# Kernel optimization log

Hardware: AMD Instinct MI355X
Metric: run time of the kernel (lower is better)

The kernel has to match this reference:

```python
import jax, jax.numpy as jnp
import numpy as np
from jax import lax

N = 10000
T_CTX = 24
HORIZON = 40
T = T_CTX + HORIZON  # 64
N_ENV = 17
COORD = 2
N_IN = N_ENV + COORD + 2  # 21
H = 128


def _lstm_cell(inp, h, c, Wih, Whh, bih, bhh):
    # torch.nn.LSTMCell gate order: input, forget, cell, output
    g = inp @ Wih.T + bih + h @ Whh.T + bhh  # [N, 4H]
    i, f, gg, o = jnp.split(g, 4, axis=1)
    c2 = jax.nn.sigmoid(f) * c + jax.nn.sigmoid(i) * jnp.tanh(gg)
    h2 = jax.nn.sigmoid(o) * jnp.tanh(c2)
    return h2, c2


def setup_inputs() -> dict:
    key = jax.random.key(0)
    ks = jax.random.split(key, 30)
    kaiming = lambda k, shp: jax.random.normal(k, shp, jnp.float32) * np.sqrt(2.0 / shp[-1]).astype(np.float32)
    u = 1.0 / np.sqrt(H).astype(np.float32)
    uni = lambda k, shp: jax.random.uniform(k, shp, jnp.float32, -u, u)
    inp = {
        'x': jax.random.uniform(ks[0], (N, T), jnp.float32),
        'coords': jax.random.normal(ks[1], (N, COORD), jnp.float32),
        'env': jax.random.normal(ks[2], (N, N_ENV, T), jnp.float32),
        'areas': jax.random.uniform(ks[3], (N,), jnp.float32),
        # encoder params (2 stacked H->H LSTM layers)
        'W_enc_in': kaiming(ks[4], (H, N_IN)),
        'enc_Wih': uni(ks[5], (2, 4 * H, H)),
        'enc_Whh': uni(ks[6], (2, 4 * H, H)),
        'enc_bih': uni(ks[7], (2, 4 * H)),
        'enc_bhh': uni(ks[8], (2, 4 * H)),
        # decoder NodeLSTM params
        'W_dec_in': kaiming(ks[9], (H, N_IN)),
        'in_Wih': uni(ks[10], (4 * H, 2 * H)),  # lstm_in takes [proj, enc_state]
        'in_Whh': uni(ks[11], (4 * H, H)),
        'in_bih': uni(ks[12], (4 * H,)),
        'in_bhh': uni(ks[13], (4 * H,)),
        'd_Wih': uni(ks[14], (4 * H, H)),
        'd_Whh': uni(ks[15], (4 * H, H)),
        'd_bih': uni(ks[16], (4 * H,)),
        'd_bhh': uni(ks[17], (4 * H,)),
        # SourceSinkMLP params
        'mlp_W1': kaiming(ks[18], (H, H + N_IN)),
        'mlp_b1': jnp.zeros((H,), jnp.float32),
        'mlp_W2': kaiming(ks[19], (2, H)),
        'mlp_b2': jnp.zeros((2,), jnp.float32),
    }
    return inp


def reference(x, coords, env, areas, W_enc_in, enc_Wih, enc_Whh, enc_bih, enc_bhh,
              W_dec_in, in_Wih, in_Whh, in_bih, in_bhh, d_Wih, d_Whh, d_bih, d_bhh,
              mlp_W1, mlp_b1, mlp_W2, mlp_b2):
    n = x.shape[0]
    areas_c = areas[:, None]
    x_seq = x.T                              # [T, N]
    env_seq = jnp.transpose(env, (2, 0, 1))  # [T, N, N_ENV]
    z = jnp.zeros((n, H), x.dtype)

    # ---- RecurrentEncoder over context steps ----
    def enc_step(carry, xs):
        h0, c0, h1, c1 = carry
        xt, et = xs
        inp = jnp.concatenate([xt[:, None], coords, et, areas_c], axis=1)  # [N, N_IN]
        proj = inp @ W_enc_in.T
        h0, c0 = _lstm_cell(proj, h0, c0, enc_Wih[0], enc_Whh[0], enc_bih[0], enc_bhh[0])
        h1, c1 = _lstm_cell(h0, h1, c1, enc_Wih[1], enc_Whh[1], enc_bih[1], enc_bhh[1])
        return (h0, c0, h1, c1), None

    (h0, c0, h1, c1), _ = lax.scan(enc_step, (z, z, z, z), (x_seq[:T_CTX], env_seq[:T_CTX]))
    enc_state = h1  # captured once in setup_states, constant over the forecast

    # ---- NodeLSTM + SourceSinkMLP rollout over the horizon ----
    def dec_step(carry, et):
        xc, h0, c0, h1, c1 = carry  # xc: [N, 1]
        inp = jnp.concatenate([xc, coords, et, areas_c], axis=1)  # [N, N_IN]
        proj = jnp.concatenate([inp @ W_dec_in.T, enc_state], axis=1)  # [N, 2H]
        h0, c0 = _lstm_cell(proj, h0, c0, in_Wih, in_Whh, in_bih, in_bhh)
        h1, c1 = _lstm_cell(h0, h1, c1, d_Wih, d_Whh, d_bih, d_bhh)
        # SourceSinkMLP
        zmid = jax.nn.leaky_relu(jnp.concatenate([h1, inp], axis=1) @ mlp_W1.T + mlp_b1)
        ss = zmid @ mlp_W2.T + mlp_b2  # [N, 2]
        source = jax.nn.sigmoid(ss[:, :1])
        sink = jax.nn.sigmoid(ss[:, 1:2]) * xc
        xn = xc + source - sink
        return (xn, h0, c0, h1, c1), xn[:, 0]

    x0 = x[:, T_CTX - 1][:, None]
    _, ys = lax.scan(dec_step, (x0, h0, c0, h1, c1), env_seq[T_CTX:T_CTX + HORIZON])
    return ys.T  # [N, HORIZON]
```

## Files before the change

### kernel.cpp

```cpp
#include <hip/hip_runtime.h>

#define NTOT  10000
#define TALL  64
#define TCTX  24
#define HOR   40
#define HH    128
#define G4    512
#define NENV  17
#define SAMP  16

typedef __attribute__((ext_vector_type(8))) short  bf16x8;
typedef __attribute__((ext_vector_type(4))) float  f32x4;
typedef unsigned short u16;

#define SEG_W0E   0
#define SEG_W0D   8192
#define SEG_WIH1  16384
#define SEG_WHH1  24576
#define SEG_DWIH  32768
#define SEG_DWHH  40960
#define SEG_M0E   49152
#define SEG_MDE   51200
#define SEG_WIHH  53248
#define SEG_W1H   61440
#define SEG_W1I   63488
#define NFRAGS    64000

#define L_WLDS  0
#define L_H0    131072
#define L_H1    135424
#define L_ZMS   139776
#define L_INPS  144128
#define L_XBLK  145408
#define L_W2L   146944
#define L_XCS   147968
#define SMEM_TOTAL 148032

__device__ __forceinline__ float sigf(float v)   { return 1.0f/(1.0f + __expf(-v)); }
__device__ __forceinline__ float tanhf_(float v) { return 1.0f - 2.0f/(__expf(2.0f*v) + 1.0f); }
__device__ __forceinline__ u16 f2bf(float f){
    unsigned int u = __float_as_uint(f);
    u += 0x7fffu + ((u >> 16) & 1u);
    return (u16)(u >> 16);
}
__device__ __forceinline__ float bf2f(u16 h){ return __uint_as_float(((unsigned int)h) << 16); }

__global__ void fold_kernel(const float* __restrict__ enc_Wih, const float* __restrict__ enc_Whh,
                            const float* __restrict__ W_enc_in,
                            const float* __restrict__ in_Wih,  const float* __restrict__ in_Whh,
                            const float* __restrict__ W_dec_in,
                            const float* __restrict__ dWih,    const float* __restrict__ dWhh,
                            const float* __restrict__ mlp_W1,  const float* __restrict__ mlp_b1,
                            const float* __restrict__ enc_bih, const float* __restrict__ enc_bhh,
                            const float* __restrict__ in_bih,  const float* __restrict__ in_bhh,
                            void* __restrict__ ws)
{
    int fid = blockIdx.x*256 + threadIdx.x;
    if (fid >= NFRAGS) return;
    const int lane = fid & 63;
    const int cc = lane & 15;
    const int kg = lane >> 4;
    float vals[8];

    if (fid < 49152) {
        int segi = fid >> 13;
        int loc  = fid & 8191;
        int gt   = loc >> 8;
        int kb   = (loc >> 6) & 3;
        int r    = gt*16 + cc;
        int k0   = kb*32 + kg*8;
        const float* src;
        switch (segi) {
            case 0: src = enc_Whh;          break;
            case 1: src = in_Whh;           break;
            case 2: src = enc_Wih + 65536;  break;
            case 3: src = enc_Whh + 65536;  break;
            case 4: src = dWih;             break;
            default: src = dWhh;            break;
        }
        #pragma unroll
        for (int j = 0; j < 8; ++j) vals[j] = src[(size_t)r*128 + k0 + j];
    } else if (fid < 53248) {
        int loc = fid - 49152;
        int which = loc >> 11; loc &= 2047;
        int gt = loc >> 6;
        int r  = gt*16 + cc;
        int k0 = kg*8;
        const float* A = which ? (in_Wih + (size_t)r*256) : (enc_Wih + (size_t)r*128);
        const float* B = which ? W_dec_in : W_enc_in;
        float bias = which ? (in_bih[r] + in_bhh[r]) : (enc_bih[r] + enc_bhh[r]);
        #pragma unroll
        for (int j = 0; j < 8; ++j) {
            int k = k0 + j;
            float v = 0.f;
            int c = (k <= 16) ? (3 + k) : (k == 17 ? 0 : (k == 18 ? 1 : (k == 19 ? 2 : (k == 20 ? 20 : -1))));
            if (k == 21) v = bias;
            else if (c >= 0) {
                float a = 0.f;
                for (int h = 0; h < HH; ++h) a = fmaf(A[h], B[h*21 + c], a);
                v = a;
            }
            vals[j] = v;
        }
    } else if (fid < 61440) {
        int loc = fid - 53248;
        int gt = loc >> 8; int kb = (loc >> 6) & 3;
        int r = gt*16 + cc; int k0 = kb*32 + kg*8;
        #pragma unroll
        for (int j = 0; j < 8; ++j) vals[j] = in_Wih[(size_t)r*256 + 128 + k0 + j];
    } else if (fid < 63488) {
        int loc = fid - 61440;
        int gt = loc >> 8; int kb = (loc >> 6) & 3;
        int r = gt*16 + cc; int k0 = kb*32 + kg*8;
        #pragma unroll
        for (int j = 0; j < 8; ++j) vals[j] = mlp_W1[(size_t)r*149 + k0 + j];
    } else {
        int loc = fid - 63488;
        int gt = loc >> 6;
        int r = gt*16 + cc; int k0 = kg*8;
        #pragma unroll
        for (int j = 0; j < 8; ++j) {
            int k = k0 + j; float v = 0.f;
            if (k <= 16)      v = mlp_W1[(size_t)r*149 + 131 + k];
            else if (k == 17) v = mlp_W1[(size_t)r*149 + 128];
            else if (k == 18) v = mlp_W1[(size_t)r*149 + 129];
            else if (k == 19) v = mlp_W1[(size_t)r*149 + 130];
            else if (k == 20) v = mlp_W1[(size_t)r*149 + 148];
            else if (k == 21) v = mlp_b1[r];
            vals[j] = v;
        }
    }
    union { uint4 u4; u16 us[8]; } pk;
    #pragma unroll
    for (int j = 0; j < 8; ++j) pk.us[j] = f2bf(vals[j]);
    *(uint4*)((char*)ws + (size_t)fid*16) = pk.u4;
}

__global__ __launch_bounds__(256, 1)
void lstm_main(const float* __restrict__ x, const float* __restrict__ coords,
               const float* __restrict__ env, const float* __restrict__ areas,
               const float* __restrict__ enc_bih, const float* __restrict__ enc_bhh,
               const float* __restrict__ dbih,   const float* __restrict__ dbhh,
               const float* __restrict__ mlp_W2, const float* __restrict__ mlp_b2,
               const void* __restrict__ ws, float* __restrict__ out)
{
    extern __shared__ char smem[];
    u16*   WLDS = (u16*)(smem + L_WLDS);
    u16*   h0s  = (u16*)(smem + L_H0);
    u16*   h1s  = (u16*)(smem + L_H1);
    u16*   zms  = (u16*)(smem + L_ZMS);
    u16*   inps = (u16*)(smem + L_INPS);
    float* xblk = (float*)(smem + L_XBLK);
    float* w2l  = (float*)(smem + L_W2L);
    float* xcs  = (float*)(smem + L_XCS);

    const int tid  = threadIdx.x;
    const int lane = tid & 63;
    const int wid  = tid >> 6;
    const int cc   = lane & 15;
    const int kg   = lane >> 4;
    const int s0   = blockIdx.x * SAMP;
    const char* wsb = (const char*)ws;

    int gmap[8];
    #pragma unroll
    for (int m = 0; m < 8; ++m) gmap[m] = ((m >> 1) << 3) + (wid << 1) + (m & 1);

    #pragma unroll 4
    for (int it = 0; it < 32; ++it) {
        int idx = it*256 + tid;
        ((uint4*)WLDS)[idx] = ((const uint4*)wsb)[idx];
    }
    for (int it = 0; it < 9; ++it) {
        int idx = it*256 + tid;
        if (idx < 2176) { h0s[idx] = 0; h1s[idx] = 0; }
    }
    #pragma unroll
    for (int rep = 0; rep < 2; ++rep) {
        int idx = rep*256 + tid;
        if (idx < 384) xblk[idx] = x[(size_t)(s0 + idx/24)*TALL + (idx % 24)];
    }
    w2l[tid] = mlp_W2[tid];

    const int sA = tid / NENV, eA = tid - sA*NENV;
    const int iB = tid + 256;
    const int sB = iB / NENV, eB = iB - sB*NENV;
    const float* envpA = env + ((size_t)(s0 + sA)*NENV + eA)*TALL;
    const float* envpB = env + ((size_t)(s0 + ((tid < 16) ? sB : 0))*NENV + ((tid < 16) ? eB : 0))*TALL;

    if (tid < SAMP) {
        inps[tid*40 + 18] = f2bf(coords[(size_t)(s0+tid)*2 + 0]);
        inps[tid*40 + 19] = f2bf(coords[(size_t)(s0+tid)*2 + 1]);
        inps[tid*40 + 20] = f2bf(areas[s0+tid]);
        inps[tid*40 + 21] = 0x3F80;
        #pragma unroll
        for (int c = 22; c < 32; ++c) inps[tid*40 + c] = 0;
    }

    bf16x8 WrA[32], WrB[32], MdB[8], W1HB[8], W1IB[2];
    float  lb1[8];
    #pragma unroll
    for (int m = 0; m < 8; ++m) {
        int gt = gmap[m];
        #pragma unroll
        for (int kb = 0; kb < 4; ++kb) {
            WrA[m*4+kb] = *(const bf16x8*)(wsb + ((size_t)(SEG_WIH1 + (gt*4+kb)*64 + lane))*16);
            WrB[m*4+kb] = *(const bf16x8*)(wsb + ((size_t)(SEG_WHH1 + (gt*4+kb)*64 + lane))*16);
        }
        MdB[m] = *(const bf16x8*)(wsb + ((size_t)(SEG_M0E + gt*64 + lane))*16);
        int grow = gt*16 + cc;
        lb1[m] = enc_bih[512 + grow] + enc_bhh[512 + grow];
    }

    float c0r[8], c1r[8];
    #pragma unroll
    for (int i = 0; i < 8; ++i) { c0r[i] = 0.f; c1r[i] = 0.f; }

    float evA = envpA[0];
    float evB = (tid < 16) ? envpB[0] : 0.f;
    __syncthreads();

    const f32x4 zero4 = {0.f, 0.f, 0.f, 0.f};

    #pragma unroll 1
    for (int t = 0; t < TCTX; ++t) {
        inps[sA*40 + eA] = f2bf(evA);
        if (tid < 16) { inps[sB*40 + eB] = f2bf(evB); inps[tid*40 + 17] = f2bf(xblk[tid*24 + t]); }
        __syncthreads();
        if (t + 1 < TALL) { evA = envpA[t+1]; if (tid < 16) evB = envpB[t+1]; }

        bf16x8 ia = *(const bf16x8*)(inps + cc*40 + kg*8);
        f32x4 acc[8];
        #pragma unroll
        for (int m = 0; m < 8; ++m)
            acc[m] = __builtin_amdgcn_mfma_f32_16x16x32_bf16(ia, MdB[m], zero4, 0, 0, 0);
        #pragma unroll
        for (int kb = 0; kb < 4; ++kb) {
            bf16x8 ha = *(const bf16x8*)(h0s + cc*136 + kb*32 + kg*8);
            #pragma unroll
            for (int m = 0; m < 8; ++m) {
                bf16x8 wb = *(const bf16x8*)((char*)WLDS + ((size_t)((gmap[m]*4+kb)*64 + lane))*16);
                acc[m] = __builtin_amdgcn_mfma_f32_16x16x32_bf16(ha, wb, acc[m], 0, 0, 0);
            }
        }
        float h2[8];
        #pragma unroll
        for (int ut = 0; ut < 2; ++ut)
        #pragma unroll
        for (int r = 0; r < 4; ++r) {
            float gi = acc[0+ut][r], gf = acc[2+ut][r], gg = acc[4+ut][r], go = acc[6+ut][r];
            float c2 = fmaf(sigf(gf), c0r[ut*4+r], sigf(gi)*tanhf_(gg));
            c0r[ut*4+r] = c2;
            h2[ut*4+r] = sigf(go)*tanhf_(c2);
        }
        __syncthreads();
        #pragma unroll
        for (int ut = 0; ut < 2; ++ut)
        #pragma unroll
        for (int r = 0; r < 4; ++r)
            h0s[(kg*4+r)*136 + wid*32 + ut*16 + cc] = f2bf(h2[ut*4+r]);
        __syncthreads();

        #pragma unroll
        for (int m = 0; m < 8; ++m) { f32x4 v = {lb1[m], lb1[m], lb1[m], lb1[m]}; acc[m] = v; }
        #pragma unroll
        for (int kb = 0; kb < 4; ++kb) {
            bf16x8 ha = *(const bf16x8*)(h0s + cc*136 + kb*32 + kg*8);
            #pragma unroll
            for (int m = 0; m < 8; ++m)
                acc[m] = __builtin_amdgcn_mfma_f32_16x16x32_bf16(ha, WrA[m*4+kb], acc[m], 0, 0, 0);
        }
        #pragma unroll
        for (int kb = 0; kb < 4; ++kb) {
            bf16x8 ha = *(const bf16x8*)(h1s + cc*136 + kb*32 + kg*8);
            #pragma unroll
            for (int m = 0; m < 8; ++m)
                acc[m] = __builtin_amdgcn_mfma_f32_16x16x32_bf16(ha, WrB[m*4+kb], acc[m], 0, 0, 0);
        }
        #pragma unroll
        for (int ut = 0; ut < 2; ++ut)
        #pragma unroll
        for (int r = 0; r < 4; ++r) {
            float gi = acc[0+ut][r], gf = acc[2+ut][r], gg = acc[4+ut][r], go = acc[6+ut][r];
            float c2 = fmaf(sigf(gf), c1r[ut*4+r], sigf(gi)*tanhf_(gg));
            c1r[ut*4+r] = c2;
            h2[ut*4+r] = sigf(go)*tanhf_(c2);
        }
        __syncthreads();
        #pragma unroll
        for (int ut = 0; ut < 2; ++ut)
        #pragma unroll
        for (int r = 0; r < 4; ++r)
            h1s[(kg*4+r)*136 + wid*32 + ut*16 + cc] = f2bf(h2[ut*4+r]);
    }

    __syncthreads();

    f32x4 baseD[8];
    #pragma unroll
    for (int m = 0; m < 8; ++m) baseD[m] = zero4;
    #pragma unroll
    for (int kb = 0; kb < 4; ++kb) {
        bf16x8 ha = *(const bf16x8*)(h1s + cc*136 + kb*32 + kg*8);
        #pragma unroll
        for (int m = 0; m < 8; ++m) {
            bf16x8 wb = *(const bf16x8*)(wsb + ((size_t)(SEG_WIHH + (gmap[m]*4+kb)*64 + lane))*16);
            baseD[m] = __builtin_amdgcn_mfma_f32_16x16x32_bf16(ha, wb, baseD[m], 0, 0, 0);
        }
    }
    #pragma unroll
    for (int m = 0; m < 8; ++m) {
        int gt = gmap[m];
        #pragma unroll
        for (int kb = 0; kb < 4; ++kb) {
            WrA[m*4+kb] = *(const bf16x8*)(wsb + ((size_t)(SEG_DWIH + (gt*4+kb)*64 + lane))*16);
            WrB[m*4+kb] = *(const bf16x8*)(wsb + ((size_t)(SEG_DWHH + (gt*4+kb)*64 + lane))*16);
        }
        MdB[m] = *(const bf16x8*)(wsb + ((size_t)(SEG_MDE + gt*64 + lane))*16);
        int grow = gt*16 + cc;
        lb1[m] = dbih[grow] + dbhh[grow];
    }
    #pragma unroll
    for (int uu = 0; uu < 2; ++uu) {
        int mt = (wid << 1) + uu;
        #pragma unroll
        for (int kb = 0; kb < 4; ++kb)
            W1HB[uu*4+kb] = *(const bf16x8*)(wsb + ((size_t)(SEG_W1H + (mt*4+kb)*64 + lane))*16);
        W1IB[uu] = *(const bf16x8*)(wsb + ((size_t)(SEG_W1I + mt*64 + lane))*16);
    }
    #pragma unroll 4
    for (int it = 0; it < 32; ++it) {
        int idx = it*256 + tid;
        ((uint4*)WLDS)[idx] = ((const uint4*)(wsb + (size_t)SEG_W0D*16))[idx];
    }
    if (tid < SAMP) {
        float xv = xblk[tid*24 + 23];
        xcs[tid] = xv;
        inps[tid*40 + 17] = f2bf(xv);
    }
    const float b20 = mlp_b2[0], b21 = mlp_b2[1];
    const int hs = lane >> 2, hq = lane & 3;
    __syncthreads();

    #pragma unroll 1
    for (int td = 0; td < HOR; ++td) {
        const int t = TCTX + td;
        inps[sA*40 + eA] = f2bf(evA);
        if (tid < 16) inps[sB*40 + eB] = f2bf(evB);
        __syncthreads();
        float xch = xcs[hs];
        if (t + 1 < TALL) { evA = envpA[t+1]; if (tid < 16) evB = envpB[t+1]; }

        bf16x8 ia = *(const bf16x8*)(inps + cc*40 + kg*8);
        f32x4 acc[8];
        #pragma unroll
        for (int m = 0; m < 8; ++m)
            acc[m] = __builtin_amdgcn_mfma_f32_16x16x32_bf16(ia, MdB[m], baseD[m], 0, 0, 0);
        #pragma unroll
        for (int kb = 0; kb < 4; ++kb) {
            bf16x8 ha = *(const bf16x8*)(h0s + cc*136 + kb*32 + kg*8);
            #pragma unroll
            for (int m = 0; m < 8; ++m) {
                bf16x8 wb = *(const bf16x8*)((char*)WLDS + ((size_t)((gmap[m]*4+kb)*64 + lane))*16);
                acc[m] = __builtin_amdgcn_mfma_f32_16x16x32_bf16(ha, wb, acc[m], 0, 0, 0);
            }
        }
        float h2[8];
        #pragma unroll
        for (int ut = 0; ut < 2; ++ut)
        #pragma unroll
        for (int r = 0; r < 4; ++r) {
            float gi = acc[0+ut][r], gf = acc[2+ut][r], gg = acc[4+ut][r], go = acc[6+ut][r];
            float c2 = fmaf(sigf(gf), c0r[ut*4+r], sigf(gi)*tanhf_(gg));
            c0r[ut*4+r] = c2;
            h2[ut*4+r] = sigf(go)*tanhf_(c2);
        }
        __syncthreads();
        #pragma unroll
        for (int ut = 0; ut < 2; ++ut)
        #pragma unroll
        for (int r = 0; r < 4; ++r)
            h0s[(kg*4+r)*136 + wid*32 + ut*16 + cc] = f2bf(h2[ut*4+r]);
        __syncthreads();

        #pragma unroll
        for (int m = 0; m < 8; ++m) { f32x4 v = {lb1[m], lb1[m], lb1[m], lb1[m]}; acc[m] = v; }
        #pragma unroll
        for (int kb = 0; kb < 4; ++kb) {
            bf16x8 ha = *(const bf16x8*)(h0s + cc*136 + kb*32 + kg*8);
            #pragma unroll
            for (int m = 0; m < 8; ++m)
                acc[m] = __builtin_amdgcn_mfma_f32_16x16x32_bf16(ha, WrA[m*4+kb], acc[m], 0, 0, 0);
        }
        #pragma unroll
        for (int kb = 0; kb < 4; ++kb) {
            bf16x8 ha = *(const bf16x8*)(h1s + cc*136 + kb*32 + kg*8);
            #pragma unroll
            for (int m = 0; m < 8; ++m)
                acc[m] = __builtin_amdgcn_mfma_f32_16x16x32_bf16(ha, WrB[m*4+kb], acc[m], 0, 0, 0);
        }
        #pragma unroll
        for (int ut = 0; ut < 2; ++ut)
        #pragma unroll
        for (int r = 0; r < 4; ++r) {
            float gi = acc[0+ut][r], gf = acc[2+ut][r], gg = acc[4+ut][r], go = acc[6+ut][r];
            float c2 = fmaf(sigf(gf), c1r[ut*4+r], sigf(gi)*tanhf_(gg));
            c1r[ut*4+r] = c2;
            h2[ut*4+r] = sigf(go)*tanhf_(c2);
        }
        __syncthreads();
        #pragma unroll
        for (int ut = 0; ut < 2; ++ut)
        #pragma unroll
        for (int r = 0; r < 4; ++r)
            h1s[(kg*4+r)*136 + wid*32 + ut*16 + cc] = f2bf(h2[ut*4+r]);
        __syncthreads();

        f32x4 macc[2];
        #pragma unroll
        for (int uu = 0; uu < 2; ++uu)
            macc[uu] = __builtin_amdgcn_mfma_f32_16x16x32_bf16(ia, W1IB[uu], zero4, 0, 0, 0);
        #pragma unroll
        for (int kb = 0; kb < 4; ++kb) {
            bf16x8 ha = *(const bf16x8*)(h1s + cc*136 + kb*32 + kg*8);
            #pragma unroll
            for (int uu = 0; uu < 2; ++uu)
                macc[uu] = __builtin_amdgcn_mfma_f32_16x16x32_bf16(ha, W1HB[uu*4+kb], macc[uu], 0, 0, 0);
        }
        #pragma unroll
        for (int uu = 0; uu < 2; ++uu)
        #pragma unroll
        for (int r = 0; r < 4; ++r) {
            float z = macc[uu][r];
            z = (z > 0.f) ? z : 0.01f*z;
            zms[(kg*4+r)*136 + wid*32 + uu*16 + cc] = f2bf(z);
        }
        __syncthreads();

        float a0 = 0.f, a1 = 0.f;
        #pragma unroll
        for (int c8 = 0; c8 < 4; ++c8) {
            bf16x8 z8 = *(const bf16x8*)(zms + hs*136 + hq*32 + c8*8);
            #pragma unroll
            for (int j = 0; j < 8; ++j) {
                float zf = bf2f((u16)z8[j]);
                int u = hq*32 + c8*8 + j;
                a0 = fmaf(zf, w2l[u], a0);
                a1 = fmaf(zf, w2l[128 + u], a1);
            }
        }
        a0 += __shfl_xor(a0, 1); a0 += __shfl_xor(a0, 2);
        a1 += __shfl_xor(a1, 1); a1 += __shfl_xor(a1, 2);
        float xn = xch + sigf(a0 + b20) - sigf(a1 + b21)*xch;
        if (wid == 0 && hq == 0) {
            xcs[hs] = xn;
            inps[hs*40 + 17] = f2bf(xn);
            out[(size_t)(s0 + hs)*HOR + td] = xn;
        }
    }
}

extern "C" void kernel_launch(void* const* d_in, const int* in_sizes, int n_in,
                              void* d_out, int out_size, void* d_ws, size_t ws_size,
                              hipStream_t stream)
{
    const float* x        = (const float*)d_in[0];
    const float* coords   = (const float*)d_in[1];
    const float* env      = (const float*)d_in[2];
    const float* areas    = (const float*)d_in[3];
    const float* W_enc_in = (const float*)d_in[4];
    const float* enc_Wih  = (const float*)d_in[5];
    const float* enc_Whh  = (const float*)d_in[6];
    const float* enc_bih  = (const float*)d_in[7];
    const float* enc_bhh  = (const float*)d_in[8];
    const float* W_dec_in = (const float*)d_in[9];
    const float* in_Wih   = (const float*)d_in[10];
    const float* in_Whh   = (const float*)d_in[11];
    const float* in_bih   = (const float*)d_in[12];
    const float* in_bhh   = (const float*)d_in[13];
    const float* dWih     = (const float*)d_in[14];
    const float* dWhh     = (const float*)d_in[15];
    const float* dbih     = (const float*)d_in[16];
    const float* dbhh     = (const float*)d_in[17];
    const float* mlp_W1   = (const float*)d_in[18];
    const float* mlp_b1   = (const float*)d_in[19];
    const float* mlp_W2   = (const float*)d_in[20];
    const float* mlp_b2   = (const float*)d_in[21];
    float* out = (float*)d_out;

    fold_kernel<<<dim3(250), dim3(256), 0, stream>>>(
        enc_Wih, enc_Whh, W_enc_in, in_Wih, in_Whh, W_dec_in,
        dWih, dWhh, mlp_W1, mlp_b1, enc_bih, enc_bhh, in_bih, in_bhh, d_ws);

    hipFuncSetAttribute((const void*)lstm_main,
                        hipFuncAttributeMaxDynamicSharedMemorySize, SMEM_TOTAL);
    lstm_main<<<dim3(NTOT/SAMP), dim3(256), SMEM_TOTAL, stream>>>(
        x, coords, env, areas, enc_bih, enc_bhh, dbih, dbhh, mlp_W2, mlp_b2, d_ws, out);
    (void)in_sizes; (void)n_in; (void)out_size; (void)ws_size;
}
```

Before: 1.200 ms.

## Split LSTM gate tiles across eight waves and double-buffer hidden states

```diff
diff --git a/kernel.cpp b/kernel.cpp
--- a/kernel.cpp
+++ b/kernel.cpp
@@ -26,15 +26,18 @@
 #define SEG_W1I   63488
 #define NFRAGS    64000
 
-#define L_WLDS  0
-#define L_H0    131072
-#define L_H1    135424
-#define L_ZMS   139776
-#define L_INPS  144128
-#define L_XBLK  145408
-#define L_W2L   146944
-#define L_XCS   147968
-#define SMEM_TOTAL 148032
+#define L_MDL   0
+#define L_W1H   32768
+#define L_W1I   65536
+#define L_BASE  73728
+#define L_H0    106496
+#define L_H1    115200
+#define L_ZMS   123904
+#define L_INPS  128256
+#define L_XBLK  129536
+#define L_W2L   131072
+#define L_XCS   132096
+#define SMEM_TOTAL 132160
 
 __device__ __forceinline__ float sigf(float v)   { return 1.0f/(1.0f + __expf(-v)); }
 __device__ __forceinline__ float tanhf_(float v) { return 1.0f - 2.0f/(__expf(2.0f*v) + 1.0f); }
@@ -136,7 +139,7 @@
     *(uint4*)((char*)ws + (size_t)fid*16) = pk.u4;
 }
 
-__global__ __launch_bounds__(256, 1)
+__global__ __launch_bounds__(512, 2)
 void lstm_main(const float* __restrict__ x, const float* __restrict__ coords,
                const float* __restrict__ env, const float* __restrict__ areas,
                const float* __restrict__ enc_bih, const float* __restrict__ enc_bhh,
@@ -145,9 +148,10 @@
                const void* __restrict__ ws, float* __restrict__ out)
 {
     extern __shared__ char smem[];
-    u16*   WLDS = (u16*)(smem + L_WLDS);
-    u16*   h0s  = (u16*)(smem + L_H0);
-    u16*   h1s  = (u16*)(smem + L_H1);
+    u16*   MdL  = (u16*)(smem + L_MDL);
+    u16*   W1Hl = (u16*)(smem + L_W1H);
+    u16*   W1Il = (u16*)(smem + L_W1I);
+    float* baseL= (float*)(smem + L_BASE);
     u16*   zms  = (u16*)(smem + L_ZMS);
     u16*   inps = (u16*)(smem + L_INPS);
     float* xblk = (float*)(smem + L_XBLK);
@@ -161,33 +165,20 @@
     const int kg   = lane >> 4;
     const int s0   = blockIdx.x * SAMP;
     const char* wsb = (const char*)ws;
-
-    int gmap[8];
+    const f32x4 zero4 = {0.f, 0.f, 0.f, 0.f};
+
     #pragma unroll
-    for (int m = 0; m < 8; ++m) gmap[m] = ((m >> 1) << 3) + (wid << 1) + (m & 1);
-
-    #pragma unroll 4
-    for (int it = 0; it < 32; ++it) {
-        int idx = it*256 + tid;
-        ((uint4*)WLDS)[idx] = ((const uint4*)wsb)[idx];
-    }
-    for (int it = 0; it < 9; ++it) {
-        int idx = it*256 + tid;
-        if (idx < 2176) { h0s[idx] = 0; h1s[idx] = 0; }
-    }
-    #pragma unroll
-    for (int rep = 0; rep < 2; ++rep) {
-        int idx = rep*256 + tid;
-        if (idx < 384) xblk[idx] = x[(size_t)(s0 + idx/24)*TALL + (idx % 24)];
-    }
-    w2l[tid] = mlp_W2[tid];
-
-    const int sA = tid / NENV, eA = tid - sA*NENV;
-    const int iB = tid + 256;
-    const int sB = iB / NENV, eB = iB - sB*NENV;
-    const float* envpA = env + ((size_t)(s0 + sA)*NENV + eA)*TALL;
-    const float* envpB = env + ((size_t)(s0 + ((tid < 16) ? sB : 0))*NENV + ((tid < 16) ? eB : 0))*TALL;
-
+    for (int i = 0; i < 4; ++i) {
+        ((uint4*)(smem + L_MDL))[i*512 + tid] = ((const uint4*)wsb)[SEG_M0E + i*512 + tid];
+        ((uint4*)(smem + L_W1H))[i*512 + tid] = ((const uint4*)wsb)[SEG_W1H + i*512 + tid];
+    }
+    ((uint4*)(smem + L_W1I))[tid] = ((const uint4*)wsb)[SEG_W1I + tid];
+    for (int i = tid; i < 2176; i += 512) {
+        ((u16*)(smem + L_H0 + 4352))[i] = 0;
+        ((u16*)(smem + L_H1 + 4352))[i] = 0;
+    }
+    if (tid < 384) xblk[tid] = x[(size_t)(s0 + tid/24)*TALL + (tid % 24)];
+    if (tid < 256) w2l[tid] = mlp_W2[tid];
     if (tid < SAMP) {
         inps[tid*40 + 18] = f2bf(coords[(size_t)(s0+tid)*2 + 0]);
         inps[tid*40 + 19] = f2bf(coords[(size_t)(s0+tid)*2 + 1]);
@@ -197,142 +188,130 @@
         for (int c = 22; c < 32; ++c) inps[tid*40 + c] = 0;
     }
 
-    bf16x8 WrA[32], WrB[32], MdB[8], W1HB[8], W1IB[2];
-    float  lb1[8];
+    const int sA = tid / NENV, eA = tid - sA*NENV;
+    const bool envth = (tid < 272);
+    const float* envp = env + ((size_t)(s0 + (envth ? sA : 0))*NENV + (envth ? eA : 0))*TALL;
+    float evA = envth ? envp[0] : 0.f;
+
+    bf16x8 W0r[16], WrA[16], WrB[16];
+    float  lb1[4];
     #pragma unroll
-    for (int m = 0; m < 8; ++m) {
-        int gt = gmap[m];
-        #pragma unroll
-        for (int kb = 0; kb < 4; ++kb) {
-            WrA[m*4+kb] = *(const bf16x8*)(wsb + ((size_t)(SEG_WIH1 + (gt*4+kb)*64 + lane))*16);
-            WrB[m*4+kb] = *(const bf16x8*)(wsb + ((size_t)(SEG_WHH1 + (gt*4+kb)*64 + lane))*16);
-        }
-        MdB[m] = *(const bf16x8*)(wsb + ((size_t)(SEG_M0E + gt*64 + lane))*16);
+    for (int g = 0; g < 4; ++g) {
+        int gt = g*8 + wid;
+        #pragma unroll
+        for (int kb = 0; kb < 4; ++kb) {
+            W0r[g*4+kb] = *(const bf16x8*)(wsb + ((size_t)(SEG_W0E  + (gt*4+kb)*64 + lane))*16);
+            WrA[g*4+kb] = *(const bf16x8*)(wsb + ((size_t)(SEG_WIH1 + (gt*4+kb)*64 + lane))*16);
+            WrB[g*4+kb] = *(const bf16x8*)(wsb + ((size_t)(SEG_WHH1 + (gt*4+kb)*64 + lane))*16);
+        }
         int grow = gt*16 + cc;
-        lb1[m] = enc_bih[512 + grow] + enc_bhh[512 + grow];
-    }
-
-    float c0r[8], c1r[8];
-    #pragma unroll
-    for (int i = 0; i < 8; ++i) { c0r[i] = 0.f; c1r[i] = 0.f; }
-
-    float evA = envpA[0];
-    float evB = (tid < 16) ? envpB[0] : 0.f;
+        lb1[g] = enc_bih[512 + grow] + enc_bhh[512 + grow];
+    }
+
+    float c0r[4] = {0.f,0.f,0.f,0.f};
+    float c1r[4] = {0.f,0.f,0.f,0.f};
     __syncthreads();
-
-    const f32x4 zero4 = {0.f, 0.f, 0.f, 0.f};
 
     #pragma unroll 1
     for (int t = 0; t < TCTX; ++t) {
-        inps[sA*40 + eA] = f2bf(evA);
-        if (tid < 16) { inps[sB*40 + eB] = f2bf(evB); inps[tid*40 + 17] = f2bf(xblk[tid*24 + t]); }
-        __syncthreads();
-        if (t + 1 < TALL) { evA = envpA[t+1]; if (tid < 16) evB = envpB[t+1]; }
+        u16* h0w = (u16*)(smem + L_H0 + (t&1)*4352);
+        u16* h0r = (u16*)(smem + L_H0 + ((t&1)^1)*4352);
+        u16* h1w = (u16*)(smem + L_H1 + (t&1)*4352);
+        u16* h1r = (u16*)(smem + L_H1 + ((t&1)^1)*4352);
+
+        if (envth)    inps[sA*40 + eA]  = f2bf(evA);
+        if (tid < 16) inps[tid*40 + 17] = f2bf(xblk[tid*24 + t]);
+        __syncthreads();
+        if (envth && t+1 < TALL) evA = envp[t+1];
 
         bf16x8 ia = *(const bf16x8*)(inps + cc*40 + kg*8);
-        f32x4 acc[8];
-        #pragma unroll
-        for (int m = 0; m < 8; ++m)
-            acc[m] = __builtin_amdgcn_mfma_f32_16x16x32_bf16(ia, MdB[m], zero4, 0, 0, 0);
-        #pragma unroll
-        for (int kb = 0; kb < 4; ++kb) {
-            bf16x8 ha = *(const bf16x8*)(h0s + cc*136 + kb*32 + kg*8);
-            #pragma unroll
-            for (int m = 0; m < 8; ++m) {
-                bf16x8 wb = *(const bf16x8*)((char*)WLDS + ((size_t)((gmap[m]*4+kb)*64 + lane))*16);
-                acc[m] = __builtin_amdgcn_mfma_f32_16x16x32_bf16(ha, wb, acc[m], 0, 0, 0);
+        f32x4 acc[4];
+        #pragma unroll
+        for (int g = 0; g < 4; ++g) {
+            bf16x8 md = *(const bf16x8*)(MdL + ((size_t)((g*8+wid)*64 + lane))*8);
+            acc[g] = __builtin_amdgcn_mfma_f32_16x16x32_bf16(ia, md, zero4, 0, 0, 0);
+        }
+        #pragma unroll
+        for (int kb = 0; kb < 4; ++kb) {
+            bf16x8 ha = *(const bf16x8*)(h0r + cc*136 + kb*32 + kg*8);
+            #pragma unroll
+            for (int g = 0; g < 4; ++g)
+                acc[g] = __builtin_amdgcn_mfma_f32_16x16x32_bf16(ha, W0r[g*4+kb], acc[g], 0, 0, 0);
+        }
+        float h2[4];
+        #pragma unroll
+        for (int r = 0; r < 4; ++r) {
+            float c2 = fmaf(sigf(acc[1][r]), c0r[r], sigf(acc[0][r])*tanhf_(acc[2][r]));
+            c0r[r] = c2;
+            h2[r] = sigf(acc[3][r])*tanhf_(c2);
+        }
+        #pragma unroll
+        for (int r = 0; r < 4; ++r)
+            h0w[(kg*4+r)*136 + wid*16 + cc] = f2bf(h2[r]);
+        __syncthreads();
+
+        #pragma unroll
+        for (int g = 0; g < 4; ++g) { f32x4 v = {lb1[g],lb1[g],lb1[g],lb1[g]}; acc[g] = v; }
+        #pragma unroll
+        for (int kb = 0; kb < 4; ++kb) {
+            bf16x8 ha = *(const bf16x8*)(h0w + cc*136 + kb*32 + kg*8);
+            #pragma unroll
+            for (int g = 0; g < 4; ++g)
+                acc[g] = __builtin_amdgcn_mfma_f32_16x16x32_bf16(ha, WrA[g*4+kb], acc[g], 0, 0, 0);
+        }
+        #pragma unroll
+        for (int kb = 0; kb < 4; ++kb) {
+            bf16x8 ha = *(const bf16x8*)(h1r + cc*136 + kb*32 + kg*8);
+            #pragma unroll
+            for (int g = 0; g < 4; ++g)
+                acc[g] = __builtin_amdgcn_mfma_f32_16x16x32_bf16(ha, WrB[g*4+kb], acc[g], 0, 0, 0);
+        }
+        #pragma unroll
+        for (int r = 0; r < 4; ++r) {
+            float c2 = fmaf(sigf(acc[1][r]), c1r[r], sigf(acc[0][r])*tanhf_(acc[2][r]));
+            c1r[r] = c2;
+            h2[r] = sigf(acc[3][r])*tanhf_(c2);
+        }
+        #pragma unroll
+        for (int r = 0; r < 4; ++r)
+            h1w[(kg*4+r)*136 + wid*16 + cc] = f2bf(h2[r]);
+    }
+
+    __syncthreads();
+
+    {
+        u16* hEnc = (u16*)(smem + L_H1 + 4352);
+        f32x4 bD[4];
+        #pragma unroll
+        for (int g = 0; g < 4; ++g) bD[g] = zero4;
+        #pragma unroll
+        for (int kb = 0; kb < 4; ++kb) {
+            bf16x8 ha = *(const bf16x8*)(hEnc + cc*136 + kb*32 + kg*8);
+            #pragma unroll
+            for (int g = 0; g < 4; ++g) {
+                bf16x8 wb = *(const bf16x8*)(wsb + ((size_t)(SEG_WIHH + ((g*8+wid)*4+kb)*64 + lane))*16);
+                bD[g] = __builtin_amdgcn_mfma_f32_16x16x32_bf16(ha, wb, bD[g], 0, 0, 0);
             }
         }
-        float h2[8];
-        #pragma unroll
-        for (int ut = 0; ut < 2; ++ut)
-        #pragma unroll
-        for (int r = 0; r < 4; ++r) {
-            float gi = acc[0+ut][r], gf = acc[2+ut][r], gg = acc[4+ut][r], go = acc[6+ut][r];
-            float c2 = fmaf(sigf(gf), c0r[ut*4+r], sigf(gi)*tanhf_(gg));
-            c0r[ut*4+r] = c2;
-            h2[ut*4+r] = sigf(go)*tanhf_(c2);
-        }
-        __syncthreads();
-        #pragma unroll
-        for (int ut = 0; ut < 2; ++ut)
-        #pragma unroll
-        for (int r = 0; r < 4; ++r)
-            h0s[(kg*4+r)*136 + wid*32 + ut*16 + cc] = f2bf(h2[ut*4+r]);
-        __syncthreads();
-
-        #pragma unroll
-        for (int m = 0; m < 8; ++m) { f32x4 v = {lb1[m], lb1[m], lb1[m], lb1[m]}; acc[m] = v; }
-        #pragma unroll
-        for (int kb = 0; kb < 4; ++kb) {
-            bf16x8 ha = *(const bf16x8*)(h0s + cc*136 + kb*32 + kg*8);
-            #pragma unroll
-            for (int m = 0; m < 8; ++m)
-                acc[m] = __builtin_amdgcn_mfma_f32_16x16x32_bf16(ha, WrA[m*4+kb], acc[m], 0, 0, 0);
-        }
-        #pragma unroll
-        for (int kb = 0; kb < 4; ++kb) {
-            bf16x8 ha = *(const bf16x8*)(h1s + cc*136 + kb*32 + kg*8);
-            #pragma unroll
-            for (int m = 0; m < 8; ++m)
-                acc[m] = __builtin_amdgcn_mfma_f32_16x16x32_bf16(ha, WrB[m*4+kb], acc[m], 0, 0, 0);
-        }
-        #pragma unroll
-        for (int ut = 0; ut < 2; ++ut)
-        #pragma unroll
-        for (int r = 0; r < 4; ++r) {
-            float gi = acc[0+ut][r], gf = acc[2+ut][r], gg = acc[4+ut][r], go = acc[6+ut][r];
-            float c2 = fmaf(sigf(gf), c1r[ut*4+r], sigf(gi)*tanhf_(gg));
-            c1r[ut*4+r] = c2;
-            h2[ut*4+r] = sigf(go)*tanhf_(c2);
-        }
-        __syncthreads();
-        #pragma unroll
-        for (int ut = 0; ut < 2; ++ut)
-        #pragma unroll
-        for (int r = 0; r < 4; ++r)
-            h1s[(kg*4+r)*136 + wid*32 + ut*16 + cc] = f2bf(h2[ut*4+r]);
-    }
-
-    __syncthreads();
-
-    f32x4 baseD[8];
+        #pragma unroll
+        for (int g = 0; g < 4; ++g)
+            *(f32x4*)(baseL + ((size_t)((wid*4+g)*64 + lane))*4) = bD[g];
+    }
     #pragma unroll
-    for (int m = 0; m < 8; ++m) baseD[m] = zero4;
+    for (int g = 0; g < 4; ++g) {
+        int gt = g*8 + wid;
+        #pragma unroll
+        for (int kb = 0; kb < 4; ++kb) {
+            W0r[g*4+kb] = *(const bf16x8*)(wsb + ((size_t)(SEG_W0D  + (gt*4+kb)*64 + lane))*16);
+            WrA[g*4+kb] = *(const bf16x8*)(wsb + ((size_t)(SEG_DWIH + (gt*4+kb)*64 + lane))*16);
+            WrB[g*4+kb] = *(const bf16x8*)(wsb + ((size_t)(SEG_DWHH + (gt*4+kb)*64 + lane))*16);
+        }
+        int grow = gt*16 + cc;
+        lb1[g] = dbih[grow] + dbhh[grow];
+    }
     #pragma unroll
-    for (int kb = 0; kb < 4; ++kb) {
-        bf16x8 ha = *(const bf16x8*)(h1s + cc*136 + kb*32 + kg*8);
-        #pragma unroll
-        for (int m = 0; m < 8; ++m) {
-            bf16x8 wb = *(const bf16x8*)(wsb + ((size_t)(SEG_WIHH + (gmap[m]*4+kb)*64 + lane))*16);
-            baseD[m] = __builtin_amdgcn_mfma_f32_16x16x32_bf16(ha, wb, baseD[m], 0, 0, 0);
-        }
-    }
-    #pragma unroll
-    for (int m = 0; m < 8; ++m) {
-        int gt = gmap[m];
-        #pragma unroll
-        for (int kb = 0; kb < 4; ++kb) {
-            WrA[m*4+kb] = *(const bf16x8*)(wsb + ((size_t)(SEG_DWIH + (gt*4+kb)*64 + lane))*16);
-            WrB[m*4+kb] = *(const bf16x8*)(wsb + ((size_t)(SEG_DWHH + (gt*4+kb)*64 + lane))*16);
-        }
-        MdB[m] = *(const bf16x8*)(wsb + ((size_t)(SEG_MDE + gt*64 + lane))*16);
-        int grow = gt*16 + cc;
-        lb1[m] = dbih[grow] + dbhh[grow];
-    }
-    #pragma unroll
-    for (int uu = 0; uu < 2; ++uu) {
-        int mt = (wid << 1) + uu;
-        #pragma unroll
-        for (int kb = 0; kb < 4; ++kb)
-            W1HB[uu*4+kb] = *(const bf16x8*)(wsb + ((size_t)(SEG_W1H + (mt*4+kb)*64 + lane))*16);
-        W1IB[uu] = *(const bf16x8*)(wsb + ((size_t)(SEG_W1I + mt*64 + lane))*16);
-    }
-    #pragma unroll 4
-    for (int it = 0; it < 32; ++it) {
-        int idx = it*256 + tid;
-        ((uint4*)WLDS)[idx] = ((const uint4*)(wsb + (size_t)SEG_W0D*16))[idx];
-    }
+    for (int i = 0; i < 4; ++i)
+        ((uint4*)(smem + L_MDL))[i*512 + tid] = ((const uint4*)wsb)[SEG_MDE + i*512 + tid];
     if (tid < SAMP) {
         float xv = xblk[tid*24 + 23];
         xcs[tid] = xv;
@@ -344,118 +323,108 @@
 
     #pragma unroll 1
     for (int td = 0; td < HOR; ++td) {
-        const int t = TCTX + td;
-        inps[sA*40 + eA] = f2bf(evA);
-        if (tid < 16) inps[sB*40 + eB] = f2bf(evB);
-        __syncthreads();
-        float xch = xcs[hs];
-        if (t + 1 < TALL) { evA = envpA[t+1]; if (tid < 16) evB = envpB[t+1]; }
+        const int q = td & 1;
+        u16* h0w = (u16*)(smem + L_H0 + q*4352);
+        u16* h0r = (u16*)(smem + L_H0 + (q^1)*4352);
+        u16* h1w = (u16*)(smem + L_H1 + q*4352);
+        u16* h1r = (u16*)(smem + L_H1 + (q^1)*4352);
+
+        if (envth) inps[sA*40 + eA] = f2bf(evA);
+        __syncthreads();
+        if (envth && TCTX+td+1 < TALL) evA = envp[TCTX+td+1];
 
         bf16x8 ia = *(const bf16x8*)(inps + cc*40 + kg*8);
-        f32x4 acc[8];
-        #pragma unroll
-        for (int m = 0; m < 8; ++m)
-            acc[m] = __builtin_amdgcn_mfma_f32_16x16x32_bf16(ia, MdB[m], baseD[m], 0, 0, 0);
-        #pragma unroll
-        for (int kb = 0; kb < 4; ++kb) {
-            bf16x8 ha = *(const bf16x8*)(h0s + cc*136 + kb*32 + kg*8);
-            #pragma unroll
-            for (int m = 0; m < 8; ++m) {
-                bf16x8 wb = *(const bf16x8*)((char*)WLDS + ((size_t)((gmap[m]*4+kb)*64 + lane))*16);
-                acc[m] = __builtin_amdgcn_mfma_f32_16x16x32_bf16(ha, wb, acc[m], 0, 0, 0);
+        f32x4 acc[4];
+        #pragma unroll
+        for (int g = 0; g < 4; ++g) {
+            f32x4 cb = *(const f32x4*)(baseL + ((size_t)((wid*4+g)*64 + lane))*4);
+            bf16x8 md = *(const bf16x8*)(MdL + ((size_t)((g*8+wid)*64 + lane))*8);
+            acc[g] = __builtin_amdgcn_mfma_f32_16x16x32_bf16(ia, md, cb, 0, 0, 0);
+        }
+        #pragma unroll
+        for (int kb = 0; kb < 4; ++kb) {
+            bf16x8 ha = *(const bf16x8*)(h0r + cc*136 + kb*32 + kg*8);
+            #pragma unroll
+            for (int g = 0; g < 4; ++g)
+                acc[g] = __builtin_amdgcn_mfma_f32_16x16x32_bf16(ha, W0r[g*4+kb], acc[g], 0, 0, 0);
+        }
+        float h2[4];
+        #pragma unroll
+        for (int r = 0; r < 4; ++r) {
+            float c2 = fmaf(sigf(acc[1][r]), c0r[r], sigf(acc[0][r])*tanhf_(acc[2][r]));
+            c0r[r] = c2;
+            h2[r] = sigf(acc[3][r])*tanhf_(c2);
+        }
+        #pragma unroll
+        for (int r = 0; r < 4; ++r)
+            h0w[(kg*4+r)*136 + wid*16 + cc] = f2bf(h2[r]);
+        __syncthreads();
+
+        #pragma unroll
+        for (int g = 0; g < 4; ++g) { f32x4 v = {lb1[g],lb1[g],lb1[g],lb1[g]}; acc[g] = v; }
+        #pragma unroll
+        for (int kb = 0; kb < 4; ++kb) {
+            bf16x8 ha = *(const bf16x8*)(h0w + cc*136 + kb*32 + kg*8);
+            #pragma unroll
+            for (int g = 0; g < 4; ++g)
+                acc[g] = __builtin_amdgcn_mfma_f32_16x16x32_bf16(ha, WrA[g*4+kb], acc[g], 0, 0, 0);
+        }
+        #pragma unroll
+        for (int kb = 0; kb < 4; ++kb) {
+            bf16x8 ha = *(const bf16x8*)(h1r + cc*136 + kb*32 + kg*8);
+            #pragma unroll
+            for (int g = 0; g < 4; ++g)
+                acc[g] = __builtin_amdgcn_mfma_f32_16x16x32_bf16(ha, WrB[g*4+kb], acc[g], 0, 0, 0);
+        }
+        #pragma unroll
+        for (int r = 0; r < 4; ++r) {
+            float c2 = fmaf(sigf(acc[1][r]), c1r[r], sigf(acc[0][r])*tanhf_(acc[2][r]));
+            c1r[r] = c2;
+            h2[r] = sigf(acc[3][r])*tanhf_(c2);
+        }
+        #pragma unroll
+        for (int r = 0; r < 4; ++r)
+            h1w[(kg*4+r)*136 + wid*16 + cc] = f2bf(h2[r]);
+        __syncthreads();
+
+        bf16x8 w1i = *(const bf16x8*)(W1Il + ((size_t)(wid*64 + lane))*8);
+        f32x4 macc = __builtin_amdgcn_mfma_f32_16x16x32_bf16(ia, w1i, zero4, 0, 0, 0);
+        #pragma unroll
+        for (int kb = 0; kb < 4; ++kb) {
+            bf16x8 ha = *(const bf16x8*)(h1w + cc*136 + kb*32 + kg*8);
+            bf16x8 wb = *(const bf16x8*)(W1Hl + ((size_t)((wid*4+kb)*64 + lane))*8);
+            macc = __builtin_amdgcn_mfma_f32_16x16x32_bf16(ha, wb, macc, 0, 0, 0);
+        }
+        #pragma unroll
+        for (int r = 0; r < 4; ++r) {
+            float z = macc[r];
+            z = (z > 0.f) ? z : 0.01f*z;
+            zms[(kg*4+r)*136 + wid*16 + cc] = f2bf(z);
+        }
+        __syncthreads();
+
+        if (wid == 0) {
+            float xch = xcs[hs];
+            float a0 = 0.f, a1 = 0.f;
+            #pragma unroll
+            for (int c8 = 0; c8 < 4; ++c8) {
+                bf16x8 z8 = *(const bf16x8*)(zms + hs*136 + hq*32 + c8*8);
+                #pragma unroll
+                for (int j = 0; j < 8; ++j) {
+                    float zf = bf2f((u16)z8[j]);
+                    int u = hq*32 + c8*8 + j;
+                    a0 = fmaf(zf, w2l[u], a0);
+                    a1 = fmaf(zf, w2l[128 + u], a1);
+                }
             }
-        }
-        float h2[8];
-        #pragma unroll
-        for (int ut = 0; ut < 2; ++ut)
-        #pragma unroll
-        for (int r = 0; r < 4; ++r) {
-            float gi = acc[0+ut][r], gf = acc[2+ut][r], gg = acc[4+ut][r], go = acc[6+ut][r];
-            float c2 = fmaf(sigf(gf), c0r[ut*4+r], sigf(gi)*tanhf_(gg));
-            c0r[ut*4+r] = c2;
-            h2[ut*4+r] = sigf(go)*tanhf_(c2);
-        }
-        __syncthreads();
-        #pragma unroll
-        for (int ut = 0; ut < 2; ++ut)
-        #pragma unroll
-        for (int r = 0; r < 4; ++r)
-            h0s[(kg*4+r)*136 + wid*32 + ut*16 + cc] = f2bf(h2[ut*4+r]);
-        __syncthreads();
-
-        #pragma unroll
-        for (int m = 0; m < 8; ++m) { f32x4 v = {lb1[m], lb1[m], lb1[m], lb1[m]}; acc[m] = v; }
-        #pragma unroll
-        for (int kb = 0; kb < 4; ++kb) {
-            bf16x8 ha = *(const bf16x8*)(h0s + cc*136 + kb*32 + kg*8);
-            #pragma unroll
-            for (int m = 0; m < 8; ++m)
-                acc[m] = __builtin_amdgcn_mfma_f32_16x16x32_bf16(ha, WrA[m*4+kb], acc[m], 0, 0, 0);
-        }
-        #pragma unroll
-        for (int kb = 0; kb < 4; ++kb) {
-            bf16x8 ha = *(const bf16x8*)(h1s + cc*136 + kb*32 + kg*8);
-            #pragma unroll
-            for (int m = 0; m < 8; ++m)
-                acc[m] = __builtin_amdgcn_mfma_f32_16x16x32_bf16(ha, WrB[m*4+kb], acc[m], 0, 0, 0);
-        }
-        #pragma unroll
-        for (int ut = 0; ut < 2; ++ut)
-        #pragma unroll
-        for (int r = 0; r < 4; ++r) {
-            float gi = acc[0+ut][r], gf = acc[2+ut][r], gg = acc[4+ut][r], go = acc[6+ut][r];
-            float c2 = fmaf(sigf(gf), c1r[ut*4+r], sigf(gi)*tanhf_(gg));
-            c1r[ut*4+r] = c2;
-            h2[ut*4+r] = sigf(go)*tanhf_(c2);
-        }
-        __syncthreads();
-        #pragma unroll
-        for (int ut = 0; ut < 2; ++ut)
-        #pragma unroll
-        for (int r = 0; r < 4; ++r)
-            h1s[(kg*4+r)*136 + wid*32 + ut*16 + cc] = f2bf(h2[ut*4+r]);
-        __syncthreads();
-
-        f32x4 macc[2];
-        #pragma unroll
-        for (int uu = 0; uu < 2; ++uu)
-            macc[uu] = __builtin_amdgcn_mfma_f32_16x16x32_bf16(ia, W1IB[uu], zero4, 0, 0, 0);
-        #pragma unroll
-        for (int kb = 0; kb < 4; ++kb) {
-            bf16x8 ha = *(const bf16x8*)(h1s + cc*136 + kb*32 + kg*8);
-            #pragma unroll
-            for (int uu = 0; uu < 2; ++uu)
-                macc[uu] = __builtin_amdgcn_mfma_f32_16x16x32_bf16(ha, W1HB[uu*4+kb], macc[uu], 0, 0, 0);
-        }
-        #pragma unroll
-        for (int uu = 0; uu < 2; ++uu)
-        #pragma unroll
-        for (int r = 0; r < 4; ++r) {
-            float z = macc[uu][r];
-            z = (z > 0.f) ? z : 0.01f*z;
-            zms[(kg*4+r)*136 + wid*32 + uu*16 + cc] = f2bf(z);
-        }
-        __syncthreads();
-
-        float a0 = 0.f, a1 = 0.f;
-        #pragma unroll
-        for (int c8 = 0; c8 < 4; ++c8) {
-            bf16x8 z8 = *(const bf16x8*)(zms + hs*136 + hq*32 + c8*8);
-            #pragma unroll
-            for (int j = 0; j < 8; ++j) {
-                float zf = bf2f((u16)z8[j]);
-                int u = hq*32 + c8*8 + j;
-                a0 = fmaf(zf, w2l[u], a0);
-                a1 = fmaf(zf, w2l[128 + u], a1);
+            a0 += __shfl_xor(a0, 1); a0 += __shfl_xor(a0, 2);
+            a1 += __shfl_xor(a1, 1); a1 += __shfl_xor(a1, 2);
+            float xn = xch + sigf(a0 + b20) - sigf(a1 + b21)*xch;
+            if (hq == 0) {
+                xcs[hs] = xn;
+                inps[hs*40 + 17] = f2bf(xn);
+                out[(size_t)(s0 + hs)*HOR + td] = xn;
             }
-        }
-        a0 += __shfl_xor(a0, 1); a0 += __shfl_xor(a0, 2);
-        a1 += __shfl_xor(a1, 1); a1 += __shfl_xor(a1, 2);
-        float xn = xch + sigf(a0 + b20) - sigf(a1 + b21)*xch;
-        if (wid == 0 && hq == 0) {
-            xcs[hs] = xn;
-            inps[hs*40 + 17] = f2bf(xn);
-            out[(size_t)(s0 + hs)*HOR + td] = xn;
         }
     }
 }
@@ -494,7 +463,7 @@
 
     hipFuncSetAttribute((const void*)lstm_main,
                         hipFuncAttributeMaxDynamicSharedMemorySize, SMEM_TOTAL);
-    lstm_main<<<dim3(NTOT/SAMP), dim3(256), SMEM_TOTAL, stream>>>(
+    lstm_main<<<dim3(NTOT/SAMP), dim3(512), SMEM_TOTAL, stream>>>(
         x, coords, env, areas, enc_bih, enc_bhh, dbih, dbhh, mlp_W2, mlp_b2, d_ws, out);
     (void)in_sizes; (void)n_in; (void)out_size; (void)ws_size;
 }
```

Measured after the change: 1.009 ms. -15.9%, faster.
